# Optimization experiments

Hardware: AMD Instinct MI355X
Metric: run time of the kernel (lower is better)

Reference implementation:

```python
import jax, jax.numpy as jnp
import numpy as np

IN_C, OUT_C = 64, 128
HID = OUT_C // 4  # 32
NEG = 0.1  # LeakyReLU slope inside MLPs


def _leaky(x, slope):
    return jnp.where(x >= 0, x, slope * x)


def gather_neighbors(x, idx):
    # x: [B,N,F], idx: [B,N',K] -> [B,N',K,F]
    return jax.vmap(lambda xb, ib: xb[ib])(x, idx)


def setup_inputs() -> dict:
    key = jax.random.key(0)
    ks = jax.random.split(key, 12)
    B, N, K = 2, 65536, 16
    x = jax.random.normal(ks[0], (B, N, IN_C), dtype=jnp.float32)
    pos = jax.random.uniform(ks[1], (B, N, 3), dtype=jnp.float32)
    neighbor_idx = jax.random.randint(ks[2], (B, N, K), 0, N)
    s = lambda fi, fo: 1.0 / np.sqrt(fi)
    W_in = jax.random.normal(ks[3], (IN_C, HID), dtype=jnp.float32) * s(IN_C, HID)
    b_in = jnp.zeros((HID,), jnp.float32)
    Wa = jax.random.normal(ks[4], (3, HID), dtype=jnp.float32) * s(3, HID)
    ba = jnp.zeros((HID,), jnp.float32)
    Wb = jax.random.normal(ks[5], (HID, HID), dtype=jnp.float32) * s(HID, HID)
    bb = jnp.zeros((HID,), jnp.float32)
    W_out = jax.random.normal(ks[6], (HID, OUT_C), dtype=jnp.float32) * s(HID, OUT_C)
    b_out = jnp.zeros((OUT_C,), jnp.float32)
    W_sc = jax.random.normal(ks[7], (IN_C, OUT_C), dtype=jnp.float32) * s(IN_C, OUT_C)
    b_sc = jnp.zeros((OUT_C,), jnp.float32)
    return dict(x=x, pos=pos, neighbor_idx=neighbor_idx,
                W_in=W_in, b_in=b_in, Wa=Wa, ba=ba, Wb=Wb, bb=bb,
                W_out=W_out, b_out=b_out, W_sc=W_sc, b_sc=b_sc)


def reference(x, pos, neighbor_idx, W_in, b_in, Wa, ba, Wb, bb, W_out, b_out, W_sc, b_sc):
    # shortcut (in_channels != out_channels -> Linear)
    residual = x @ W_sc + b_sc                      # [B,N,OUT]
    h = _leaky(x @ W_in + b_in, NEG)                # [B,N,HID]
    # PointConv: per-edge weights from relative positions
    nbr_pos = gather_neighbors(pos, neighbor_idx)   # [B,N,K,3]
    rel = pos[:, :, None, :] - nbr_pos              # [B,N,K,3]
    w = _leaky(rel @ Wa + ba, NEG) @ Wb + bb        # [B,N,K,HID]
    hg = gather_neighbors(h, neighbor_idx)          # [B,N,K,HID]
    conv = jnp.sum(w * hg, axis=2)                  # [B,N,HID]
    out = conv @ W_out + b_out                      # [B,N,OUT]
    return _leaky(out + residual, 0.01)             # F.leaky_relu default slope
```

## Files before the change

kernel.cpp:

```cpp
#include <hip/hip_runtime.h>
#include <hip/hip_bf16.h>

#define IN_C 64
#define OUT_C 128
#define HID 32
#define KNB 16

typedef __attribute__((ext_vector_type(8))) short short8;
typedef __attribute__((ext_vector_type(4))) float f32x4;

__device__ __forceinline__ float leaky(float v, float s) { return fmaxf(v, s * v); }

__device__ __forceinline__ unsigned bf16u(float f) {
    __hip_bfloat16 h = __float2bfloat16(f);
    return (unsigned)*reinterpret_cast<unsigned short*>(&h);
}
__device__ __forceinline__ short bf16s(float f) {
    __hip_bfloat16 h = __float2bfloat16(f);
    return *reinterpret_cast<short*>(&h);
}

__global__ __launch_bounds__(256) void pack_kernel(
    const float* __restrict__ pos, const float* __restrict__ Wout,
    const float* __restrict__ Wsc, float4* __restrict__ pos4,
    short* __restrict__ pk, int P)
{
    int t = blockIdx.x * 256 + threadIdx.x;
    if (t < 1536) {
        int ks = t >> 9, rem = t & 511;
        int nt = rem >> 6, g = (rem >> 4) & 3, n = rem & 15;
        int col = nt * 16 + n;
        short8 v;
        #pragma unroll
        for (int e = 0; e < 8; ++e) {
            int row = ks * 32 + 8 * g + e;
            float f = (row < 32) ? Wout[row * OUT_C + col]
                                 : Wsc[(row - 32) * OUT_C + col];
            v[e] = bf16s(f);
        }
        *(short8*)(pk + (long)t * 8) = v;
    }
    if (t < P) {
        float4 v;
        v.x = pos[3L * t + 0]; v.y = pos[3L * t + 1];
        v.z = pos[3L * t + 2]; v.w = 0.f;
        pos4[t] = v;
    }
}

__global__ __launch_bounds__(256) void hid_mfma(
    const float* __restrict__ x, const float* __restrict__ Win,
    const float* __restrict__ bin, unsigned* __restrict__ h2, int P)
{
    int lane = threadIdx.x & 63;
    int widx = __builtin_amdgcn_readfirstlane(threadIdx.x >> 6);
    int wavebase = (blockIdx.x * 4 + widx) * 16;
    if (wavebase >= P) return;
    int n = lane & 15, g = lane >> 4;

    short8 bfr[2][2];
    #pragma unroll
    for (int ks = 0; ks < 2; ++ks)
        #pragma unroll
        for (int nt = 0; nt < 2; ++nt)
            #pragma unroll
            for (int e = 0; e < 8; ++e)
                bfr[ks][nt][e] = bf16s(Win[(ks * 32 + 8 * g + e) * HID + nt * 16 + n]);

    float bv0 = bin[n], bv1 = bin[16 + n];

    const float* xr = x + (long)(wavebase + n) * IN_C;
    short8 a[2];
    #pragma unroll
    for (int ks = 0; ks < 2; ++ks) {
        float4 v0 = *(const float4*)(xr + ks * 32 + 8 * g);
        float4 v1 = *(const float4*)(xr + ks * 32 + 8 * g + 4);
        a[ks][0] = bf16s(v0.x); a[ks][1] = bf16s(v0.y);
        a[ks][2] = bf16s(v0.z); a[ks][3] = bf16s(v0.w);
        a[ks][4] = bf16s(v1.x); a[ks][5] = bf16s(v1.y);
        a[ks][6] = bf16s(v1.z); a[ks][7] = bf16s(v1.w);
    }

    f32x4 acc0 = { bv0, bv0, bv0, bv0 };
    f32x4 acc1 = { bv1, bv1, bv1, bv1 };
    acc0 = __builtin_amdgcn_mfma_f32_16x16x32_bf16(a[0], bfr[0][0], acc0, 0, 0, 0);
    acc0 = __builtin_amdgcn_mfma_f32_16x16x32_bf16(a[1], bfr[1][0], acc0, 0, 0, 0);
    acc1 = __builtin_amdgcn_mfma_f32_16x16x32_bf16(a[0], bfr[0][1], acc1, 0, 0, 0);
    acc1 = __builtin_amdgcn_mfma_f32_16x16x32_bf16(a[1], bfr[1][1], acc1, 0, 0, 0);

    #pragma unroll
    for (int r = 0; r < 4; ++r) {
        unsigned lo = bf16u(leaky(acc0[r], 0.1f));
        unsigned hi = bf16u(leaky(acc1[r], 0.1f));
        h2[(long)(wavebase + 4 * g + r) * 16 + n] = (hi << 16) | lo;
    }
}

__global__ __launch_bounds__(128) __attribute__((amdgpu_waves_per_eu(3, 4)))
void edgeout_mfma(
    const float* __restrict__ x, const float4* __restrict__ pos4,
    const int* __restrict__ nbr, const unsigned* __restrict__ h2,
    const float* __restrict__ Wa, const float* __restrict__ ba,
    const float* __restrict__ Wb, const float* __restrict__ bb,
    const short* __restrict__ pk, const float* __restrict__ bout,
    const float* __restrict__ bsc, float* __restrict__ out, int N, int P)
{
    __shared__ float cbuf[2][32 * 17];

    int tid = threadIdx.x;
    int lane = tid & 63;
    int widx = __builtin_amdgcn_readfirstlane(tid >> 6);
    int n = lane & 15, g = lane >> 4;
    int wavebase = (blockIdx.x * 2 + widx) * 16;
    if (wavebase >= P) return;
    long pbase = (wavebase >= N) ? (long)N : 0;

    float waX[8], waY[8], waZ[8], bav[8];
    #pragma unroll
    for (int e = 0; e < 8; ++e) {
        int k = 8 * g + e;
        waX[e] = Wa[k]; waY[e] = Wa[HID + k]; waZ[e] = Wa[2 * HID + k];
        bav[e] = ba[k];
    }
    short8 wb0, wb1;
    #pragma unroll
    for (int e = 0; e < 8; ++e) {
        int k = 8 * g + e;
        wb0[e] = bf16s(Wb[k * HID + n]);
        wb1[e] = bf16s(Wb[k * HID + 16 + n]);
    }
    float bb0 = bb[n], bb1 = bb[16 + n];
    float* cb = cbuf[widx];

    const float* xr = x + (long)(wavebase + n) * IN_C;
    float4 u0 = *(const float4*)(xr + 8 * g);
    float4 u1 = *(const float4*)(xr + 8 * g + 4);
    float4 u2 = *(const float4*)(xr + 32 + 8 * g);
    float4 u3 = *(const float4*)(xr + 32 + 8 * g + 4);

    int4  qv[KNB]; int qs[KNB];
    float4 pp[KNB], pq[KNB];
    unsigned hv[KNB][4];

#define IDX(i) {                                                        \
        const int* nr = nbr + (long)(wavebase + (i)) * KNB;             \
        qv[i] = *(const int4*)(nr + 4 * g);                             \
        qs[i] = nr[n]; }
#define GATHER(i) {                                                     \
        pp[i] = pos4[wavebase + (i)];                                   \
        pq[i] = pos4[pbase + qs[i]];                                    \
        hv[i][0] = h2[(pbase + qv[i].x) * 16 + n];                      \
        hv[i][1] = h2[(pbase + qv[i].y) * 16 + n];                      \
        hv[i][2] = h2[(pbase + qv[i].z) * 16 + n];                      \
        hv[i][3] = h2[(pbase + qv[i].w) * 16 + n]; }

    #pragma unroll
    for (int pt = 0; pt < KNB; ++pt) {
        if (pt == 0) { IDX(0) IDX(1) GATHER(0) }
        if (pt + 2 < KNB) IDX(pt + 2)
        if (pt + 1 < KNB) GATHER(pt + 1)

        float rx = pp[pt].x - pq[pt].x;
        float ry = pp[pt].y - pq[pt].y;
        float rz = pp[pt].z - pq[pt].z;

        short8 af;
        #pragma unroll
        for (int e = 0; e < 8; ++e) {
            float tv = fmaf(rx, waX[e], fmaf(ry, waY[e], fmaf(rz, waZ[e], bav[e])));
            af[e] = bf16s(leaky(tv, 0.1f));
        }

        f32x4 w0 = { bb0, bb0, bb0, bb0 };
        f32x4 w1 = { bb1, bb1, bb1, bb1 };
        w0 = __builtin_amdgcn_mfma_f32_16x16x32_bf16(af, wb0, w0, 0, 0, 0);
        w1 = __builtin_amdgcn_mfma_f32_16x16x32_bf16(af, wb1, w1, 0, 0, 0);

        float hA0 = __uint_as_float(hv[pt][0] << 16), hB0 = __uint_as_float(hv[pt][0] & 0xffff0000u);
        float hA1 = __uint_as_float(hv[pt][1] << 16), hB1 = __uint_as_float(hv[pt][1] & 0xffff0000u);
        float hA2 = __uint_as_float(hv[pt][2] << 16), hB2 = __uint_as_float(hv[pt][2] & 0xffff0000u);
        float hA3 = __uint_as_float(hv[pt][3] << 16), hB3 = __uint_as_float(hv[pt][3] & 0xffff0000u);

        float pa = fmaf(w0[0], hA0, fmaf(w0[1], hA1, fmaf(w0[2], hA2, w0[3] * hA3)));
        float pb = fmaf(w1[0], hB0, fmaf(w1[1], hB1, fmaf(w1[2], hB2, w1[3] * hB3)));
        pa += __shfl_xor(pa, 16, 64);  pa += __shfl_xor(pa, 32, 64);
        pb += __shfl_xor(pb, 16, 64);  pb += __shfl_xor(pb, 32, 64);

        if (g == 0)      cb[n * 17 + pt]        = pa;
        else if (g == 1) cb[(n + 16) * 17 + pt] = pb;
    }
#undef IDX
#undef GATHER

    asm volatile("s_waitcnt lgkmcnt(0)" ::: "memory");

    short8 a0, a1, a2;
    #pragma unroll
    for (int e = 0; e < 8; ++e)
        a0[e] = bf16s(cb[(8 * g + e) * 17 + n]);
    a1[0] = bf16s(u0.x); a1[1] = bf16s(u0.y); a1[2] = bf16s(u0.z); a1[3] = bf16s(u0.w);
    a1[4] = bf16s(u1.x); a1[5] = bf16s(u1.y); a1[6] = bf16s(u1.z); a1[7] = bf16s(u1.w);
    a2[0] = bf16s(u2.x); a2[1] = bf16s(u2.y); a2[2] = bf16s(u2.z); a2[3] = bf16s(u2.w);
    a2[4] = bf16s(u3.x); a2[5] = bf16s(u3.y); a2[6] = bf16s(u3.z); a2[7] = bf16s(u3.w);

    #pragma unroll 2
    for (int nt = 0; nt < 8; ++nt) {
        short8 b0 = *(const short8*)(pk + ((long)(0 * 8 + nt) * 64 + lane) * 8);
        short8 b1 = *(const short8*)(pk + ((long)(1 * 8 + nt) * 64 + lane) * 8);
        short8 b2 = *(const short8*)(pk + ((long)(2 * 8 + nt) * 64 + lane) * 8);
        int o = nt * 16 + n;
        float bv = bout[o] + bsc[o];
        f32x4 acc = { bv, bv, bv, bv };
        acc = __builtin_amdgcn_mfma_f32_16x16x32_bf16(a0, b0, acc, 0, 0, 0);
        acc = __builtin_amdgcn_mfma_f32_16x16x32_bf16(a1, b1, acc, 0, 0, 0);
        acc = __builtin_amdgcn_mfma_f32_16x16x32_bf16(a2, b2, acc, 0, 0, 0);
        #pragma unroll
        for (int r = 0; r < 4; ++r)
            out[(long)(wavebase + 4 * g + r) * OUT_C + o] = leaky(acc[r], 0.01f);
    }
}

extern "C" void kernel_launch(void* const* d_in, const int* in_sizes, int n_in,
                              void* d_out, int out_size, void* d_ws, size_t ws_size,
                              hipStream_t stream) {
    const float* x    = (const float*)d_in[0];
    const float* pos  = (const float*)d_in[1];
    const int*   nbr  = (const int*)d_in[2];
    const float* Win  = (const float*)d_in[3];
    const float* bin  = (const float*)d_in[4];
    const float* Wa   = (const float*)d_in[5];
    const float* ba   = (const float*)d_in[6];
    const float* Wb   = (const float*)d_in[7];
    const float* bb   = (const float*)d_in[8];
    const float* Wout = (const float*)d_in[9];
    const float* bout = (const float*)d_in[10];
    const float* Wsc  = (const float*)d_in[11];
    const float* bsc  = (const float*)d_in[12];
    float* out = (float*)d_out;

    int P = in_sizes[0] / IN_C;
    int N = P / 2;

    unsigned* h2  = (unsigned*)d_ws;
    float4*  pos4 = (float4*)((char*)d_ws + (size_t)P * 64);
    short*   pk   = (short*)((char*)d_ws + (size_t)P * 64 + (size_t)P * 16);

    pack_kernel<<<(P + 255) / 256, 256, 0, stream>>>(pos, Wout, Wsc, pos4, pk, P);
    hid_mfma<<<(P + 63) / 64, 256, 0, stream>>>(x, Win, bin, h2, P);
    edgeout_mfma<<<(P + 31) / 32, 128, 0, stream>>>(
        x, pos4, nbr, h2, Wa, ba, Wb, bb, pk, bout, bsc, out, N, P);
}
```

Baseline: 67.28 us.

## Fuse pack kernel into hid_mfma and deepen neighbor gather prefetch

Merges the pos/weight packing work into the hid_mfma kernel so one launch is removed. The edge kernel now prefetches neighbor indices three points ahead and gathers two ahead, so more gather latency is hidden. The waves_per_eu attribute is dropped, which lets the compiler use more registers for the deeper pipeline at the cost of occupancy. One caveat: hid_mfma runs (P+63)/64 blocks of 256 threads, so tg reaches about 4P and still covers P. The early-return path for waves past the end sits after the packing code, which keeps the fused kernel correct.

Result: faster. 63.61 us (-5.5%).

```diff
diff --git a/kernel.cpp b/kernel.cpp
--- a/kernel.cpp
+++ b/kernel.cpp
@@ -20,38 +20,36 @@
     return *reinterpret_cast<short*>(&h);
 }
 
-__global__ __launch_bounds__(256) void pack_kernel(
-    const float* __restrict__ pos, const float* __restrict__ Wout,
-    const float* __restrict__ Wsc, float4* __restrict__ pos4,
+__global__ __launch_bounds__(256) void hid_mfma(
+    const float* __restrict__ x, const float* __restrict__ Win,
+    const float* __restrict__ bin, const float* __restrict__ pos,
+    const float* __restrict__ Wout, const float* __restrict__ Wsc,
+    unsigned* __restrict__ h2, float4* __restrict__ pos4,
     short* __restrict__ pk, int P)
 {
-    int t = blockIdx.x * 256 + threadIdx.x;
-    if (t < 1536) {
-        int ks = t >> 9, rem = t & 511;
-        int nt = rem >> 6, g = (rem >> 4) & 3, n = rem & 15;
-        int col = nt * 16 + n;
+    int tg = blockIdx.x * 256 + (int)threadIdx.x;
+
+    if (tg < P) {
+        float4 v;
+        v.x = pos[3L * tg + 0]; v.y = pos[3L * tg + 1];
+        v.z = pos[3L * tg + 2]; v.w = 0.f;
+        pos4[tg] = v;
+    }
+    if (tg < 1536) {
+        int ks = tg >> 9, rem = tg & 511;
+        int nt = rem >> 6, g2 = (rem >> 4) & 3, n2 = rem & 15;
+        int col = nt * 16 + n2;
         short8 v;
         #pragma unroll
         for (int e = 0; e < 8; ++e) {
-            int row = ks * 32 + 8 * g + e;
+            int row = ks * 32 + 8 * g2 + e;
             float f = (row < 32) ? Wout[row * OUT_C + col]
                                  : Wsc[(row - 32) * OUT_C + col];
             v[e] = bf16s(f);
         }
-        *(short8*)(pk + (long)t * 8) = v;
-    }
-    if (t < P) {
-        float4 v;
-        v.x = pos[3L * t + 0]; v.y = pos[3L * t + 1];
-        v.z = pos[3L * t + 2]; v.w = 0.f;
-        pos4[t] = v;
-    }
-}
-
-__global__ __launch_bounds__(256) void hid_mfma(
-    const float* __restrict__ x, const float* __restrict__ Win,
-    const float* __restrict__ bin, unsigned* __restrict__ h2, int P)
-{
+        *(short8*)(pk + (long)tg * 8) = v;
+    }
+
     int lane = threadIdx.x & 63;
     int widx = __builtin_amdgcn_readfirstlane(threadIdx.x >> 6);
     int wavebase = (blockIdx.x * 4 + widx) * 16;
@@ -96,7 +94,7 @@
     }
 }
 
-__global__ __launch_bounds__(128) __attribute__((amdgpu_waves_per_eu(3, 4)))
+__global__ __launch_bounds__(128)
 void edgeout_mfma(
     const float* __restrict__ x, const float4* __restrict__ pos4,
     const int* __restrict__ nbr, const unsigned* __restrict__ h2,
@@ -156,9 +154,9 @@
 
     #pragma unroll
     for (int pt = 0; pt < KNB; ++pt) {
-        if (pt == 0) { IDX(0) IDX(1) GATHER(0) }
-        if (pt + 2 < KNB) IDX(pt + 2)
-        if (pt + 1 < KNB) GATHER(pt + 1)
+        if (pt == 0) { IDX(0) IDX(1) IDX(2) GATHER(0) GATHER(1) }
+        if (pt + 3 < KNB) IDX(pt + 3)
+        if (pt + 2 < KNB) GATHER(pt + 2)
 
         float rx = pp[pt].x - pq[pt].x;
         float ry = pp[pt].y - pq[pt].y;
@@ -245,8 +243,8 @@
     float4*  pos4 = (float4*)((char*)d_ws + (size_t)P * 64);
     short*   pk   = (short*)((char*)d_ws + (size_t)P * 64 + (size_t)P * 16);
 
-    pack_kernel<<<(P + 255) / 256, 256, 0, stream>>>(pos, Wout, Wsc, pos4, pk, P);
-    hid_mfma<<<(P + 63) / 64, 256, 0, stream>>>(x, Win, bin, h2, P);
+    hid_mfma<<<(P + 63) / 64, 256, 0, stream>>>(
+        x, Win, bin, pos, Wout, Wsc, h2, pos4, pk, P);
     edgeout_mfma<<<(P + 31) / 32, 128, 0, stream>>>(
         x, pos4, nbr, h2, Wa, ba, Wb, bb, pk, bout, bsc, out, N, P);
 }
```
